# Performance work log

Hardware: AMD Instinct MI355X
Metric: run time of the kernel (lower is better)

The kernel has to match this reference:

```python
import jax, jax.numpy as jnp
import numpy as np

N, E, D = 50000, 800000, 128

def setup_inputs() -> dict:
    key = jax.random.key(0)
    ks = jax.random.split(key, 8)
    x = jax.random.normal(ks[0], (N, D), dtype=jnp.float32)
    edge_index = jax.random.randint(ks[1], (2, E), 0, N, dtype=jnp.int64)
    s2 = 1.0 / np.sqrt(2 * D)
    s4 = 1.0 / np.sqrt(4 * D)
    s1 = 1.0 / np.sqrt(D)
    pre_W = jax.random.uniform(ks[2], (2 * D, D), jnp.float32, -s2, s2)   # pre MLP (1 layer)
    pre_b = jax.random.uniform(ks[3], (D,), jnp.float32, -s2, s2)
    post_W = jax.random.uniform(ks[4], (4 * D, D), jnp.float32, -s4, s4)  # post MLP (1 layer)
    post_b = jax.random.uniform(ks[5], (D,), jnp.float32, -s4, s4)
    lin_W = jax.random.uniform(ks[6], (D, D), jnp.float32, -s1, s1)       # final projection
    lin_b = jax.random.uniform(ks[7], (D,), jnp.float32, -s1, s1)
    return {"x": x, "edge_index": edge_index, "pre_W": pre_W, "pre_b": pre_b,
            "post_W": post_W, "post_b": post_b, "lin_W": lin_W, "lin_b": lin_b}

def reference(x, edge_index, pre_W, pre_b, post_W, post_b, lin_W, lin_b):
    n = x.shape[0]
    src, dst = edge_index[0], edge_index[1]  # message flows src -> dst (source_to_target)
    # message: pre MLP on concat(x_i=target, x_j=source)  [E, 2D] -> [E, D]
    h = jnp.concatenate([x[dst], x[src]], axis=-1)
    m = h @ pre_W + pre_b
    # multi-aggregator scatter: mean, max, sum over destination nodes
    s = jax.ops.segment_sum(m, dst, num_segments=n)
    cnt = jax.ops.segment_sum(jnp.ones((m.shape[0], 1), m.dtype), dst, num_segments=n)
    mean = s / jnp.maximum(cnt, 1.0)
    mx = jax.ops.segment_max(m, dst, num_segments=n)
    mx = jnp.where(cnt > 0, mx, 0.0)  # empty segments -> 0 (PyG fill)
    aggr = jnp.concatenate([mean, mx, s], axis=-1)  # order: mean, max, sum
    # update: post MLP on concat(x, aggr)  [N, 4D] -> [N, D], then final lin
    out = jnp.concatenate([x, aggr], axis=-1) @ post_W + post_b
    out = out @ lin_W + lin_b
    # wrapper: relu + dropout (eval mode -> identity)
    return jax.nn.relu(out)
```

## Files before the change

### kernel.cpp

```cpp
#include <hip/hip_runtime.h>
#include <float.h>

#define NN 50000
#define EE 800000
#define NBKT 196
#define T1 4096
#define CAP2 8192

typedef __attribute__((ext_vector_type(8))) short bf16x8;
typedef __attribute__((ext_vector_type(4))) float f32x4;
typedef unsigned short u16;
typedef unsigned int u32;

__device__ __forceinline__ u16 f2bf(float f) {
  u32 u = __builtin_bit_cast(u32, f);
  u32 r = (u + 0x7fffu + ((u >> 16) & 1u)) >> 16;
  return (u16)r;
}
__device__ __forceinline__ float bflo(u32 q) { return __builtin_bit_cast(float, q << 16); }
__device__ __forceinline__ float bfhi(u32 q) { return __builtin_bit_cast(float, q & 0xffff0000u); }

__global__ __launch_bounds__(256) void k_prep(const float* __restrict__ post_W,
    const float* __restrict__ post_b, const float* __restrict__ lin_W,
    const float* __restrict__ lin_b, const float* __restrict__ pre_W,
    u16* __restrict__ WpT, u16* __restrict__ WpqT, float* __restrict__ bp) {
  int idx = blockIdx.x * 256 + threadIdx.x;
  if (idx < 512 * 128) {
    int i = idx >> 7, j = idx & 127;
    float s = 0.f;
#pragma unroll 8
    for (int c = 0; c < 128; c++) s += post_W[i * 128 + c] * lin_W[c * 128 + j];
    WpT[j * 512 + i] = f2bf(s);
  } else if (idx < 512 * 128 + 256 * 128) {
    int u = idx - 512 * 128;
    int j = u >> 7, k = u & 127;
    float v = (j < 128) ? pre_W[k * 128 + j] : pre_W[(128 + k) * 128 + (j - 128)];
    WpqT[j * 128 + k] = f2bf(v);
  } else if (idx < 512 * 128 + 256 * 128 + 128) {
    int j = idx - (512 * 128 + 256 * 128);
    float s = lin_b[j];
    for (int c = 0; c < 128; c++) s += post_b[c] * lin_W[c * 128 + j];
    bp[j] = s;
  }
}

__global__ __launch_bounds__(256) void k_convert_x(const float* __restrict__ x,
                                                   u16* __restrict__ Xcat) {
  int tid = blockIdx.x * 256 + threadIdx.x;
  if (tid >= NN * 16) return;
  int row = tid >> 4;
  int col = (tid & 15) << 3;
  const float4 v0 = *(const float4*)(x + (size_t)row * 128 + col);
  const float4 v1 = *(const float4*)(x + (size_t)row * 128 + col + 4);
  u16 tmp[8] = {f2bf(v0.x), f2bf(v0.y), f2bf(v0.z), f2bf(v0.w),
                f2bf(v1.x), f2bf(v1.y), f2bf(v1.z), f2bf(v1.w)};
  *(bf16x8*)(Xcat + (size_t)row * 512 + col) = *(bf16x8*)tmp;
}

template <int KTOT, int LDA>
__device__ __forceinline__ void stage_tiles(const u16* __restrict__ A,
    const u16* __restrict__ BT, int row0, int n0, int k0,
    u16* __restrict__ As, u16* __restrict__ Bs, int t) {
#pragma unroll
  for (int it = 0; it < 4; ++it) {
    int c = t + it * 256;
    int row = c >> 3, ch = c & 7;
    int gr = row0 + row;
    bf16x8 v = {};
    if (gr < NN) v = *(const bf16x8*)(A + (size_t)gr * LDA + k0 + (ch << 3));
    *(bf16x8*)(As + row * 64 + ((ch ^ (row & 7)) << 3)) = v;
  }
#pragma unroll
  for (int it = 0; it < 4; ++it) {
    int c = t + it * 256;
    int n = c >> 3, ch = c & 7;
    bf16x8 v = *(const bf16x8*)(BT + (size_t)(n0 + n) * KTOT + k0 + (ch << 3));
    *(bf16x8*)(Bs + n * 64 + ((ch ^ (n & 7)) << 3)) = v;
  }
}

__device__ __forceinline__ bf16x8 ld_frag(const u16* __restrict__ S, int rowbase,
                                          int kk, int lane) {
  int r = rowbase + (lane & 15);
  int chunk = (kk >> 3) + (lane >> 4);
  int sw = chunk ^ (r & 7);
  return *(const bf16x8*)(S + r * 64 + (sw << 3));
}

__global__ __launch_bounds__(256) void k_gemm_pq(const u16* __restrict__ Xcat,
    const u16* __restrict__ WpqT, u16* __restrict__ PQb) {
  __shared__ u16 As[128 * 64];
  __shared__ u16 Bs[128 * 64];
  const int t = threadIdx.x;
  const int lane = t & 63, wid = t >> 6;
  const int wr = wid >> 1, wc = wid & 1;
  const int row0 = blockIdx.x * 128;
  const int n0 = blockIdx.y * 128;
  f32x4 acc[4][4] = {};
  for (int k0 = 0; k0 < 128; k0 += 64) {
    stage_tiles<128, 512>(Xcat, WpqT, row0, n0, k0, As, Bs, t);
    __syncthreads();
#pragma unroll
    for (int kk = 0; kk < 64; kk += 32) {
      bf16x8 af[4], bg[4];
#pragma unroll
      for (int m = 0; m < 4; ++m) af[m] = ld_frag(As, wr * 64 + m * 16, kk, lane);
#pragma unroll
      for (int n = 0; n < 4; ++n) bg[n] = ld_frag(Bs, wc * 64 + n * 16, kk, lane);
#pragma unroll
      for (int m = 0; m < 4; ++m)
#pragma unroll
        for (int n = 0; n < 4; ++n)
          acc[m][n] = __builtin_amdgcn_mfma_f32_16x16x32_bf16(af[m], bg[n], acc[m][n], 0, 0, 0);
    }
    __syncthreads();
  }
#pragma unroll
  for (int m = 0; m < 4; ++m) {
    int rb = row0 + wr * 64 + m * 16 + ((lane >> 4) << 2);
#pragma unroll
    for (int n = 0; n < 4; ++n) {
      int col = n0 + wc * 64 + n * 16 + (lane & 15);
#pragma unroll
      for (int r = 0; r < 4; ++r) {
        int row = rb + r;
        if (row < NN) PQb[(size_t)row * 256 + col] = f2bf(acc[m][n][r]);
      }
    }
  }
}

__global__ __launch_bounds__(256) void k_gemm_out(const u16* __restrict__ Xcat,
    const u16* __restrict__ WpT, const float* __restrict__ bp,
    float* __restrict__ out) {
  __shared__ u16 As[128 * 64];
  __shared__ u16 Bs[128 * 64];
  const int t = threadIdx.x;
  const int lane = t & 63, wid = t >> 6;
  const int wr = wid >> 1, wc = wid & 1;
  const int row0 = blockIdx.x * 128;
  f32x4 acc[4][4] = {};
  for (int k0 = 0; k0 < 512; k0 += 64) {
    stage_tiles<512, 512>(Xcat, WpT, row0, 0, k0, As, Bs, t);
    __syncthreads();
#pragma unroll
    for (int kk = 0; kk < 64; kk += 32) {
      bf16x8 af[4], bg[4];
#pragma unroll
      for (int m = 0; m < 4; ++m) af[m] = ld_frag(As, wr * 64 + m * 16, kk, lane);
#pragma unroll
      for (int n = 0; n < 4; ++n) bg[n] = ld_frag(Bs, wc * 64 + n * 16, kk, lane);
#pragma unroll
      for (int m = 0; m < 4; ++m)
#pragma unroll
        for (int n = 0; n < 4; ++n)
          acc[m][n] = __builtin_amdgcn_mfma_f32_16x16x32_bf16(af[m], bg[n], acc[m][n], 0, 0, 0);
    }
    __syncthreads();
  }
#pragma unroll
  for (int m = 0; m < 4; ++m) {
    int rb = row0 + wr * 64 + m * 16 + ((lane >> 4) << 2);
#pragma unroll
    for (int n = 0; n < 4; ++n) {
      int col = wc * 64 + n * 16 + (lane & 15);
      float bias = bp[col];
#pragma unroll
      for (int r = 0; r < 4; ++r) {
        int row = rb + r;
        if (row < NN) out[(size_t)row * 128 + col] = fmaxf(acc[m][n][r] + bias, 0.f);
      }
    }
  }
}

__global__ void k_zero256(int* __restrict__ bucket_cnt) {
  bucket_cnt[threadIdx.x] = 0;
}

__global__ __launch_bounds__(256) void k_bucketcnt(const int* __restrict__ ei,
                                                   int* __restrict__ bucket_cnt) {
  __shared__ int hist[256];
  const int t = threadIdx.x;
  hist[t] = 0;
  __syncthreads();
  const int e0 = blockIdx.x * T1;
  const int ec = min(T1, EE - e0);
  for (int j = t; j < ec; j += 256) atomicAdd(&hist[ei[EE + e0 + j] >> 8], 1);
  __syncthreads();
  if (hist[t]) atomicAdd(&bucket_cnt[t], hist[t]);
}

__global__ void k_scanbucket(const int* __restrict__ bucket_cnt,
                             int* __restrict__ bucket_base,
                             int* __restrict__ bucket_cursor) {
  __shared__ int sd[256];
  int t = threadIdx.x;
  int v = (t < NBKT) ? bucket_cnt[t] : 0;
  sd[t] = v;
  __syncthreads();
  for (int s = 1; s < 256; s <<= 1) {
    int tv = (t >= s) ? sd[t - s] : 0;
    __syncthreads();
    sd[t] += tv;
    __syncthreads();
  }
  int excl = sd[t] - v;
  bucket_base[t] = excl;
  bucket_cursor[t] = excl;
}

__global__ __launch_bounds__(256) void k_bucket(const int* __restrict__ ei,
    int* __restrict__ bucket_cursor, u32* __restrict__ ebuf) {
  __shared__ u32 tilebuf[T1];
  __shared__ u32 gpos[T1];
  __shared__ int hist[256], scan_[256], runbase[256], ctr[256];
  const int t = threadIdx.x;
  const int e0 = blockIdx.x * T1;
  const int ecount = min(T1, EE - e0);
  hist[t] = 0;
  __syncthreads();
  u32 myp[16];
  int myb[16];
#pragma unroll
  for (int k = 0; k < 16; ++k) {
    int idx = t + k * 256;
    myp[k] = 0; myb[k] = 0;
    if (idx < ecount) {
      int e = e0 + idx;
      int s = ei[e], d = ei[EE + e];
      myp[k] = ((u32)d << 16) | (u32)s;
      int b = d >> 8;
      myb[k] = b;
      atomicAdd(&hist[b], 1);
    }
  }
  __syncthreads();
  int v = hist[t];
  scan_[t] = v;
  __syncthreads();
  for (int s_ = 1; s_ < 256; s_ <<= 1) {
    int tv = (t >= s_) ? scan_[t - s_] : 0;
    __syncthreads();
    scan_[t] += tv;
    __syncthreads();
  }
  int excl = scan_[t] - v;
  __syncthreads();
  scan_[t] = excl;
  ctr[t] = 0;
  if (v > 0) runbase[t] = atomicAdd(&bucket_cursor[t], v);
  __syncthreads();
#pragma unroll
  for (int k = 0; k < 16; ++k) {
    int idx = t + k * 256;
    if (idx < ecount) {
      int b = myb[k];
      int l = atomicAdd(&ctr[b], 1);
      int slot = scan_[b] + l;
      tilebuf[slot] = myp[k];
      gpos[slot] = (u32)(runbase[b] + l);
    }
  }
  __syncthreads();
  for (int j = t; j < ecount; j += 256) ebuf[gpos[j]] = tilebuf[j];
}

__global__ __launch_bounds__(256) void k_sortbucket(const u32* __restrict__ ebuf,
    const int* __restrict__ bucket_base, int* __restrict__ row_ptr,
    u16* __restrict__ csr_src) {
  __shared__ u16 sorted[CAP2];
  __shared__ int hist[256], scan_[256], ctr[256];
  const int b = blockIdx.x;
  const int t = threadIdx.x;
  const int base = bucket_base[b];
  const int end = bucket_base[b + 1];
  const int count = end - base;
  hist[t] = 0;
  __syncthreads();
  for (int j = t; j < count; j += 256) atomicAdd(&hist[(ebuf[base + j] >> 16) & 255], 1);
  __syncthreads();
  int v = hist[t];
  scan_[t] = v;
  __syncthreads();
  for (int s_ = 1; s_ < 256; s_ <<= 1) {
    int tv = (t >= s_) ? scan_[t - s_] : 0;
    __syncthreads();
    scan_[t] += tv;
    __syncthreads();
  }
  int excl = scan_[t] - v;
  __syncthreads();
  scan_[t] = excl;
  ctr[t] = 0;
  int node = b * 256 + t;
  if (node < NN) row_ptr[node] = base + excl;
  if (b == NBKT - 1 && t == 0) row_ptr[NN] = EE;
  __syncthreads();
  if (count <= CAP2) {
    for (int j = t; j < count; j += 256) {
      u32 p = ebuf[base + j];
      int ln = (p >> 16) & 255;
      int l = atomicAdd(&ctr[ln], 1);
      sorted[scan_[ln] + l] = (u16)(p & 0xffffu);
    }
    __syncthreads();
    for (int j = t; j < count; j += 256) csr_src[base + j] = sorted[j];
  } else {
    for (int j = t; j < count; j += 256) {
      u32 p = ebuf[base + j];
      int ln = (p >> 16) & 255;
      int l = atomicAdd(&ctr[ln], 1);
      csr_src[base + scan_[ln] + l] = (u16)(p & 0xffffu);
    }
  }
}

__global__ __launch_bounds__(256) void k_aggr(const u16* __restrict__ PQb,
    const float* __restrict__ pre_b, const int* __restrict__ row_ptr,
    const u16* __restrict__ csr_src, u16* __restrict__ Xcat) {
  int wid = (blockIdx.x * 256 + threadIdx.x) >> 6;
  int lane = threadIdx.x & 63;
  if (wid >= NN) return;
  int r0 = row_ptr[wid], r1 = row_ptr[wid + 1];
  int c = lane * 2;
  const u16* Qbase = PQb + 128 + c;
  float sx = 0.f, sy = 0.f, mxx = -FLT_MAX, mxy = -FLT_MAX;
  int i = r0;
  for (; i + 16 <= r1; i += 16) {
    int s[16];
#pragma unroll
    for (int k = 0; k < 16; ++k) s[k] = csr_src[i + k];
    u32 q[16];
#pragma unroll
    for (int k = 0; k < 16; ++k) q[k] = *(const u32*)(Qbase + (size_t)s[k] * 256);
#pragma unroll
    for (int k = 0; k < 16; ++k) {
      float qx = bflo(q[k]), qy = bfhi(q[k]);
      sx += qx; sy += qy;
      mxx = fmaxf(mxx, qx); mxy = fmaxf(mxy, qy);
    }
  }
  if (i + 8 <= r1) {
    int s[8];
#pragma unroll
    for (int k = 0; k < 8; ++k) s[k] = csr_src[i + k];
    u32 q[8];
#pragma unroll
    for (int k = 0; k < 8; ++k) q[k] = *(const u32*)(Qbase + (size_t)s[k] * 256);
#pragma unroll
    for (int k = 0; k < 8; ++k) {
      float qx = bflo(q[k]), qy = bfhi(q[k]);
      sx += qx; sy += qy;
      mxx = fmaxf(mxx, qx); mxy = fmaxf(mxy, qy);
    }
    i += 8;
  }
  if (i + 4 <= r1) {
    int s[4];
#pragma unroll
    for (int k = 0; k < 4; ++k) s[k] = csr_src[i + k];
    u32 q[4];
#pragma unroll
    for (int k = 0; k < 4; ++k) q[k] = *(const u32*)(Qbase + (size_t)s[k] * 256);
#pragma unroll
    for (int k = 0; k < 4; ++k) {
      float qx = bflo(q[k]), qy = bfhi(q[k]);
      sx += qx; sy += qy;
      mxx = fmaxf(mxx, qx); mxy = fmaxf(mxy, qy);
    }
    i += 4;
  }
  for (; i < r1; ++i) {
    int s = csr_src[i];
    u32 q = *(const u32*)(Qbase + (size_t)s * 256);
    float qx = bflo(q), qy = bfhi(q);
    sx += qx; sy += qy;
    mxx = fmaxf(mxx, qx); mxy = fmaxf(mxy, qy);
  }
  u32 pu = *(const u32*)(PQb + (size_t)wid * 256 + c);
  float2 b = *(const float2*)(pre_b + c);
  float px = bflo(pu) + b.x;
  float py = bfhi(pu) + b.y;
  int deg = r1 - r0;
  float vm_x = 0.f, vm_y = 0.f, vx_x = 0.f, vx_y = 0.f, vs_x = 0.f, vs_y = 0.f;
  if (deg > 0) {
    float inv = 1.0f / (float)deg;
    vm_x = px + sx * inv;          vm_y = py + sy * inv;
    vx_x = px + mxx;               vx_y = py + mxy;
    vs_x = (float)deg * px + sx;   vs_y = (float)deg * py + sy;
  }
  u16* arow = Xcat + (size_t)wid * 512 + 128;
  *(u32*)(arow + c)       = (u32)f2bf(vm_x) | ((u32)f2bf(vm_y) << 16);
  *(u32*)(arow + 128 + c) = (u32)f2bf(vx_x) | ((u32)f2bf(vx_y) << 16);
  *(u32*)(arow + 256 + c) = (u32)f2bf(vs_x) | ((u32)f2bf(vs_y) << 16);
}

extern "C" void kernel_launch(void* const* d_in, const int* in_sizes, int n_in,
                              void* d_out, int out_size, void* d_ws, size_t ws_size,
                              hipStream_t stream) {
  const float* x      = (const float*)d_in[0];
  const int*   ei     = (const int*)d_in[1];
  const float* pre_W  = (const float*)d_in[2];
  const float* pre_b  = (const float*)d_in[3];
  const float* post_W = (const float*)d_in[4];
  const float* post_b = (const float*)d_in[5];
  const float* lin_W  = (const float*)d_in[6];
  const float* lin_b  = (const float*)d_in[7];
  float* out = (float*)d_out;

  char* ws = (char*)d_ws;
  size_t off = 0;
  auto alloc = [&](size_t bytes) { size_t o = off; off = (off + bytes + 511) & ~(size_t)511; return o; };
  u16*   Xcat    = (u16*)(ws + alloc((size_t)NN * 512 * 2));
  u16*   PQb     = (u16*)(ws + alloc((size_t)NN * 256 * 2));
  u16*   WpT     = (u16*)(ws + alloc(128 * 512 * 2));
  u16*   WpqT    = (u16*)(ws + alloc(256 * 128 * 2));
  float* bp      = (float*)(ws + alloc(128 * 4));
  int*   row_ptr = (int*)(ws + alloc((size_t)(NN + 1) * 4));
  int*   bucket_cnt    = (int*)(ws + alloc(256 * 4));
  int*   bucket_base   = (int*)(ws + alloc(257 * 4));
  int*   bucket_cursor = (int*)(ws + alloc(256 * 4));
  u32*   ebuf    = (u32*)(ws + alloc((size_t)EE * 4));
  u16*   csr_src = (u16*)(ws + alloc((size_t)EE * 2));
  (void)ws_size; (void)in_sizes; (void)n_in; (void)out_size;

  const int NB_M = (NN + 127) / 128;
  const int NB_T = (EE + T1 - 1) / T1;

  k_prep<<<(512 * 128 + 256 * 128 + 128 + 255) / 256, 256, 0, stream>>>(
      post_W, post_b, lin_W, lin_b, pre_W, WpT, WpqT, bp);
  k_convert_x<<<(NN * 16 + 255) / 256, 256, 0, stream>>>(x, Xcat);
  k_zero256<<<1, 256, 0, stream>>>(bucket_cnt);
  k_bucketcnt<<<NB_T, 256, 0, stream>>>(ei, bucket_cnt);
  k_gemm_pq<<<dim3(NB_M, 2), 256, 0, stream>>>(Xcat, WpqT, PQb);
  k_scanbucket<<<1, 256, 0, stream>>>(bucket_cnt, bucket_base, bucket_cursor);
  k_bucket<<<NB_T, 256, 0, stream>>>(ei, bucket_cursor, ebuf);
  k_sortbucket<<<NBKT, 256, 0, stream>>>(ebuf, bucket_base, row_ptr, csr_src);
  k_aggr<<<(NN * 64 + 255) / 256, 256, 0, stream>>>(PQb, pre_b, row_ptr, csr_src, Xcat);
  k_gemm_out<<<NB_M, 256, 0, stream>>>(Xcat, WpT, bp, out);
}
```

Measured before the change: 126.6 us.

## Fuse setup kernels, use per-tile bucket partials, smaller out-GEMM tiles, scalarize CSR indices

Measured after the change: 127.0 us. Within noise of the previous version (+0.3%).

```diff
diff --git a/kernel.cpp b/kernel.cpp
--- a/kernel.cpp
+++ b/kernel.cpp
@@ -7,6 +7,11 @@
 #define T1 4096
 #define CAP2 8192
 
+#define NB_CONV 3125
+#define NB_PREP 385
+#define NB_CNT  196
+#define NB_SETUP (NB_CONV + NB_PREP + NB_CNT)
+
 typedef __attribute__((ext_vector_type(8))) short bf16x8;
 typedef __attribute__((ext_vector_type(4))) float f32x4;
 typedef unsigned short u16;
@@ -20,49 +25,188 @@
 __device__ __forceinline__ float bflo(u32 q) { return __builtin_bit_cast(float, q << 16); }
 __device__ __forceinline__ float bfhi(u32 q) { return __builtin_bit_cast(float, q & 0xffff0000u); }
 
-__global__ __launch_bounds__(256) void k_prep(const float* __restrict__ post_W,
-    const float* __restrict__ post_b, const float* __restrict__ lin_W,
-    const float* __restrict__ lin_b, const float* __restrict__ pre_W,
-    u16* __restrict__ WpT, u16* __restrict__ WpqT, float* __restrict__ bp) {
-  int idx = blockIdx.x * 256 + threadIdx.x;
-  if (idx < 512 * 128) {
-    int i = idx >> 7, j = idx & 127;
-    float s = 0.f;
+__global__ __launch_bounds__(256) void k_setup(const float* __restrict__ x,
+    const float* __restrict__ post_W, const float* __restrict__ post_b,
+    const float* __restrict__ lin_W, const float* __restrict__ lin_b,
+    const float* __restrict__ pre_W, const int* __restrict__ ei,
+    u16* __restrict__ Xcat, u16* __restrict__ WpT, u16* __restrict__ WpqT,
+    float* __restrict__ bp, int* __restrict__ bucket_part) {
+  __shared__ int hist[256];
+  const int bid = blockIdx.x;
+  const int t = threadIdx.x;
+  if (bid < NB_CONV) {
+    int tid = bid * 256 + t;
+    int row = tid >> 4;
+    int col = (tid & 15) << 3;
+    const float4 v0 = *(const float4*)(x + (size_t)row * 128 + col);
+    const float4 v1 = *(const float4*)(x + (size_t)row * 128 + col + 4);
+    u16 tmp[8] = {f2bf(v0.x), f2bf(v0.y), f2bf(v0.z), f2bf(v0.w),
+                  f2bf(v1.x), f2bf(v1.y), f2bf(v1.z), f2bf(v1.w)};
+    *(bf16x8*)(Xcat + (size_t)row * 512 + col) = *(bf16x8*)tmp;
+  } else if (bid < NB_CONV + NB_PREP) {
+    int idx = (bid - NB_CONV) * 256 + t;
+    if (idx < 512 * 128) {
+      int i = idx >> 7, j = idx & 127;
+      float s = 0.f;
 #pragma unroll 8
-    for (int c = 0; c < 128; c++) s += post_W[i * 128 + c] * lin_W[c * 128 + j];
-    WpT[j * 512 + i] = f2bf(s);
-  } else if (idx < 512 * 128 + 256 * 128) {
-    int u = idx - 512 * 128;
-    int j = u >> 7, k = u & 127;
-    float v = (j < 128) ? pre_W[k * 128 + j] : pre_W[(128 + k) * 128 + (j - 128)];
-    WpqT[j * 128 + k] = f2bf(v);
-  } else if (idx < 512 * 128 + 256 * 128 + 128) {
-    int j = idx - (512 * 128 + 256 * 128);
-    float s = lin_b[j];
-    for (int c = 0; c < 128; c++) s += post_b[c] * lin_W[c * 128 + j];
-    bp[j] = s;
-  }
-}
-
-__global__ __launch_bounds__(256) void k_convert_x(const float* __restrict__ x,
-                                                   u16* __restrict__ Xcat) {
-  int tid = blockIdx.x * 256 + threadIdx.x;
-  if (tid >= NN * 16) return;
-  int row = tid >> 4;
-  int col = (tid & 15) << 3;
-  const float4 v0 = *(const float4*)(x + (size_t)row * 128 + col);
-  const float4 v1 = *(const float4*)(x + (size_t)row * 128 + col + 4);
-  u16 tmp[8] = {f2bf(v0.x), f2bf(v0.y), f2bf(v0.z), f2bf(v0.w),
-                f2bf(v1.x), f2bf(v1.y), f2bf(v1.z), f2bf(v1.w)};
-  *(bf16x8*)(Xcat + (size_t)row * 512 + col) = *(bf16x8*)tmp;
-}
-
-template <int KTOT, int LDA>
+      for (int c = 0; c < 128; c++) s += post_W[i * 128 + c] * lin_W[c * 128 + j];
+      WpT[j * 512 + i] = f2bf(s);
+    } else if (idx < 512 * 128 + 256 * 128) {
+      int u = idx - 512 * 128;
+      int j = u >> 7, k = u & 127;
+      float v = (j < 128) ? pre_W[k * 128 + j] : pre_W[(128 + k) * 128 + (j - 128)];
+      WpqT[j * 128 + k] = f2bf(v);
+    } else if (idx < 512 * 128 + 256 * 128 + 128) {
+      int j = idx - (512 * 128 + 256 * 128);
+      float s = lin_b[j];
+      for (int c = 0; c < 128; c++) s += post_b[c] * lin_W[c * 128 + j];
+      bp[j] = s;
+    }
+  } else {
+    int tile = bid - (NB_CONV + NB_PREP);
+    hist[t] = 0;
+    __syncthreads();
+    const int e0 = tile * T1;
+    const int ec = min(T1, EE - e0);
+    for (int j = t; j < ec; j += 256) atomicAdd(&hist[ei[EE + e0 + j] >> 8], 1);
+    __syncthreads();
+    bucket_part[tile * 256 + t] = hist[t];
+  }
+}
+
+__global__ void k_scanbucket(const int* __restrict__ bucket_part,
+                             int* __restrict__ bucket_base,
+                             int* __restrict__ bucket_cursor) {
+  __shared__ int sd[256];
+  int t = threadIdx.x;
+  int v = 0;
+#pragma unroll 4
+  for (int b = 0; b < NB_CNT; ++b) v += bucket_part[b * 256 + t];
+  sd[t] = v;
+  __syncthreads();
+  for (int s = 1; s < 256; s <<= 1) {
+    int tv = (t >= s) ? sd[t - s] : 0;
+    __syncthreads();
+    sd[t] += tv;
+    __syncthreads();
+  }
+  int excl = sd[t] - v;
+  bucket_base[t] = excl;
+  bucket_cursor[t] = excl;
+}
+
+__global__ __launch_bounds__(256) void k_bucket(const int* __restrict__ ei,
+    int* __restrict__ bucket_cursor, u32* __restrict__ ebuf) {
+  __shared__ u32 tilebuf[T1];
+  __shared__ u32 gpos[T1];
+  __shared__ int hist[256], scan_[256], runbase[256], ctr[256];
+  const int t = threadIdx.x;
+  const int e0 = blockIdx.x * T1;
+  const int ecount = min(T1, EE - e0);
+  hist[t] = 0;
+  __syncthreads();
+  u32 myp[16];
+  int myb[16];
+#pragma unroll
+  for (int k = 0; k < 16; ++k) {
+    int idx = t + k * 256;
+    myp[k] = 0; myb[k] = 0;
+    if (idx < ecount) {
+      int e = e0 + idx;
+      int s = ei[e], d = ei[EE + e];
+      myp[k] = ((u32)d << 16) | (u32)s;
+      int b = d >> 8;
+      myb[k] = b;
+      atomicAdd(&hist[b], 1);
+    }
+  }
+  __syncthreads();
+  int v = hist[t];
+  scan_[t] = v;
+  __syncthreads();
+  for (int s_ = 1; s_ < 256; s_ <<= 1) {
+    int tv = (t >= s_) ? scan_[t - s_] : 0;
+    __syncthreads();
+    scan_[t] += tv;
+    __syncthreads();
+  }
+  int excl = scan_[t] - v;
+  __syncthreads();
+  scan_[t] = excl;
+  ctr[t] = 0;
+  if (v > 0) runbase[t] = atomicAdd(&bucket_cursor[t], v);
+  __syncthreads();
+#pragma unroll
+  for (int k = 0; k < 16; ++k) {
+    int idx = t + k * 256;
+    if (idx < ecount) {
+      int b = myb[k];
+      int l = atomicAdd(&ctr[b], 1);
+      int slot = scan_[b] + l;
+      tilebuf[slot] = myp[k];
+      gpos[slot] = (u32)(runbase[b] + l);
+    }
+  }
+  __syncthreads();
+  for (int j = t; j < ecount; j += 256) ebuf[gpos[j]] = tilebuf[j];
+}
+
+__global__ __launch_bounds__(256) void k_sortbucket(const u32* __restrict__ ebuf,
+    const int* __restrict__ bucket_base, int* __restrict__ row_ptr,
+    u16* __restrict__ csr_src) {
+  __shared__ u16 sorted[CAP2];
+  __shared__ int hist[256], scan_[256], ctr[256];
+  const int b = blockIdx.x;
+  const int t = threadIdx.x;
+  const int base = bucket_base[b];
+  const int end = bucket_base[b + 1];
+  const int count = end - base;
+  hist[t] = 0;
+  __syncthreads();
+  for (int j = t; j < count; j += 256) atomicAdd(&hist[(ebuf[base + j] >> 16) & 255], 1);
+  __syncthreads();
+  int v = hist[t];
+  scan_[t] = v;
+  __syncthreads();
+  for (int s_ = 1; s_ < 256; s_ <<= 1) {
+    int tv = (t >= s_) ? scan_[t - s_] : 0;
+    __syncthreads();
+    scan_[t] += tv;
+    __syncthreads();
+  }
+  int excl = scan_[t] - v;
+  __syncthreads();
+  scan_[t] = excl;
+  ctr[t] = 0;
+  int node = b * 256 + t;
+  if (node < NN) row_ptr[node] = base + excl;
+  if (b == NBKT - 1 && t == 0) row_ptr[NN] = EE;
+  __syncthreads();
+  if (count <= CAP2) {
+    for (int j = t; j < count; j += 256) {
+      u32 p = ebuf[base + j];
+      int ln = (p >> 16) & 255;
+      int l = atomicAdd(&ctr[ln], 1);
+      sorted[scan_[ln] + l] = (u16)(p & 0xffffu);
+    }
+    __syncthreads();
+    for (int j = t; j < count; j += 256) csr_src[base + j] = sorted[j];
+  } else {
+    for (int j = t; j < count; j += 256) {
+      u32 p = ebuf[base + j];
+      int ln = (p >> 16) & 255;
+      int l = atomicAdd(&ctr[ln], 1);
+      csr_src[base + scan_[ln] + l] = (u16)(p & 0xffffu);
+    }
+  }
+}
+
+template <int KTOT, int LDA, int AROWS>
 __device__ __forceinline__ void stage_tiles(const u16* __restrict__ A,
     const u16* __restrict__ BT, int row0, int n0, int k0,
     u16* __restrict__ As, u16* __restrict__ Bs, int t) {
 #pragma unroll
-  for (int it = 0; it < 4; ++it) {
+  for (int it = 0; it < AROWS / 32; ++it) {
     int c = t + it * 256;
     int row = c >> 3, ch = c & 7;
     int gr = row0 + row;
@@ -98,7 +242,7 @@
   const int n0 = blockIdx.y * 128;
   f32x4 acc[4][4] = {};
   for (int k0 = 0; k0 < 128; k0 += 64) {
-    stage_tiles<128, 512>(Xcat, WpqT, row0, n0, k0, As, Bs, t);
+    stage_tiles<128, 512, 128>(Xcat, WpqT, row0, n0, k0, As, Bs, t);
     __syncthreads();
 #pragma unroll
     for (int kk = 0; kk < 64; kk += 32) {
@@ -133,25 +277,25 @@
 __global__ __launch_bounds__(256) void k_gemm_out(const u16* __restrict__ Xcat,
     const u16* __restrict__ WpT, const float* __restrict__ bp,
     float* __restrict__ out) {
-  __shared__ u16 As[128 * 64];
+  __shared__ u16 As[64 * 64];
   __shared__ u16 Bs[128 * 64];
   const int t = threadIdx.x;
   const int lane = t & 63, wid = t >> 6;
   const int wr = wid >> 1, wc = wid & 1;
-  const int row0 = blockIdx.x * 128;
-  f32x4 acc[4][4] = {};
+  const int row0 = blockIdx.x * 64;
+  f32x4 acc[2][4] = {};
   for (int k0 = 0; k0 < 512; k0 += 64) {
-    stage_tiles<512, 512>(Xcat, WpT, row0, 0, k0, As, Bs, t);
+    stage_tiles<512, 512, 64>(Xcat, WpT, row0, 0, k0, As, Bs, t);
     __syncthreads();
 #pragma unroll
     for (int kk = 0; kk < 64; kk += 32) {
-      bf16x8 af[4], bg[4];
-#pragma unroll
-      for (int m = 0; m < 4; ++m) af[m] = ld_frag(As, wr * 64 + m * 16, kk, lane);
+      bf16x8 af[2], bg[4];
+#pragma unroll
+      for (int m = 0; m < 2; ++m) af[m] = ld_frag(As, wr * 32 + m * 16, kk, lane);
 #pragma unroll
       for (int n = 0; n < 4; ++n) bg[n] = ld_frag(Bs, wc * 64 + n * 16, kk, lane);
 #pragma unroll
-      for (int m = 0; m < 4; ++m)
+      for (int m = 0; m < 2; ++m)
 #pragma unroll
         for (int n = 0; n < 4; ++n)
           acc[m][n] = __builtin_amdgcn_mfma_f32_16x16x32_bf16(af[m], bg[n], acc[m][n], 0, 0, 0);
@@ -159,8 +303,8 @@
     __syncthreads();
   }
 #pragma unroll
-  for (int m = 0; m < 4; ++m) {
-    int rb = row0 + wr * 64 + m * 16 + ((lane >> 4) << 2);
+  for (int m = 0; m < 2; ++m) {
+    int rb = row0 + wr * 32 + m * 16 + ((lane >> 4) << 2);
 #pragma unroll
     for (int n = 0; n < 4; ++n) {
       int col = wc * 64 + n * 16 + (lane & 15);
@@ -170,148 +314,6 @@
         int row = rb + r;
         if (row < NN) out[(size_t)row * 128 + col] = fmaxf(acc[m][n][r] + bias, 0.f);
       }
-    }
-  }
-}
-
-__global__ void k_zero256(int* __restrict__ bucket_cnt) {
-  bucket_cnt[threadIdx.x] = 0;
-}
-
-__global__ __launch_bounds__(256) void k_bucketcnt(const int* __restrict__ ei,
-                                                   int* __restrict__ bucket_cnt) {
-  __shared__ int hist[256];
-  const int t = threadIdx.x;
-  hist[t] = 0;
-  __syncthreads();
-  const int e0 = blockIdx.x * T1;
-  const int ec = min(T1, EE - e0);
-  for (int j = t; j < ec; j += 256) atomicAdd(&hist[ei[EE + e0 + j] >> 8], 1);
-  __syncthreads();
-  if (hist[t]) atomicAdd(&bucket_cnt[t], hist[t]);
-}
-
-__global__ void k_scanbucket(const int* __restrict__ bucket_cnt,
-                             int* __restrict__ bucket_base,
-                             int* __restrict__ bucket_cursor) {
-  __shared__ int sd[256];
-  int t = threadIdx.x;
-  int v = (t < NBKT) ? bucket_cnt[t] : 0;
-  sd[t] = v;
-  __syncthreads();
-  for (int s = 1; s < 256; s <<= 1) {
-    int tv = (t >= s) ? sd[t - s] : 0;
-    __syncthreads();
-    sd[t] += tv;
-    __syncthreads();
-  }
-  int excl = sd[t] - v;
-  bucket_base[t] = excl;
-  bucket_cursor[t] = excl;
-}
-
-__global__ __launch_bounds__(256) void k_bucket(const int* __restrict__ ei,
-    int* __restrict__ bucket_cursor, u32* __restrict__ ebuf) {
-  __shared__ u32 tilebuf[T1];
-  __shared__ u32 gpos[T1];
-  __shared__ int hist[256], scan_[256], runbase[256], ctr[256];
-  const int t = threadIdx.x;
-  const int e0 = blockIdx.x * T1;
-  const int ecount = min(T1, EE - e0);
-  hist[t] = 0;
-  __syncthreads();
-  u32 myp[16];
-  int myb[16];
-#pragma unroll
-  for (int k = 0; k < 16; ++k) {
-    int idx = t + k * 256;
-    myp[k] = 0; myb[k] = 0;
-    if (idx < ecount) {
-      int e = e0 + idx;
-      int s = ei[e], d = ei[EE + e];
-      myp[k] = ((u32)d << 16) | (u32)s;
-      int b = d >> 8;
-      myb[k] = b;
-      atomicAdd(&hist[b], 1);
-    }
-  }
-  __syncthreads();
-  int v = hist[t];
-  scan_[t] = v;
-  __syncthreads();
-  for (int s_ = 1; s_ < 256; s_ <<= 1) {
-    int tv = (t >= s_) ? scan_[t - s_] : 0;
-    __syncthreads();
-    scan_[t] += tv;
-    __syncthreads();
-  }
-  int excl = scan_[t] - v;
-  __syncthreads();
-  scan_[t] = excl;
-  ctr[t] = 0;
-  if (v > 0) runbase[t] = atomicAdd(&bucket_cursor[t], v);
-  __syncthreads();
-#pragma unroll
-  for (int k = 0; k < 16; ++k) {
-    int idx = t + k * 256;
-    if (idx < ecount) {
-      int b = myb[k];
-      int l = atomicAdd(&ctr[b], 1);
-      int slot = scan_[b] + l;
-      tilebuf[slot] = myp[k];
-      gpos[slot] = (u32)(runbase[b] + l);
-    }
-  }
-  __syncthreads();
-  for (int j = t; j < ecount; j += 256) ebuf[gpos[j]] = tilebuf[j];
-}
-
-__global__ __launch_bounds__(256) void k_sortbucket(const u32* __restrict__ ebuf,
-    const int* __restrict__ bucket_base, int* __restrict__ row_ptr,
-    u16* __restrict__ csr_src) {
-  __shared__ u16 sorted[CAP2];
-  __shared__ int hist[256], scan_[256], ctr[256];
-  const int b = blockIdx.x;
-  const int t = threadIdx.x;
-  const int base = bucket_base[b];
-  const int end = bucket_base[b + 1];
-  const int count = end - base;
-  hist[t] = 0;
-  __syncthreads();
-  for (int j = t; j < count; j += 256) atomicAdd(&hist[(ebuf[base + j] >> 16) & 255], 1);
-  __syncthreads();
-  int v = hist[t];
-  scan_[t] = v;
-  __syncthreads();
-  for (int s_ = 1; s_ < 256; s_ <<= 1) {
-    int tv = (t >= s_) ? scan_[t - s_] : 0;
-    __syncthreads();
-    scan_[t] += tv;
-    __syncthreads();
-  }
-  int excl = scan_[t] - v;
-  __syncthreads();
-  scan_[t] = excl;
-  ctr[t] = 0;
-  int node = b * 256 + t;
-  if (node < NN) row_ptr[node] = base + excl;
-  if (b == NBKT - 1 && t == 0) row_ptr[NN] = EE;
-  __syncthreads();
-  if (count <= CAP2) {
-    for (int j = t; j < count; j += 256) {
-      u32 p = ebuf[base + j];
-      int ln = (p >> 16) & 255;
-      int l = atomicAdd(&ctr[ln], 1);
-      sorted[scan_[ln] + l] = (u16)(p & 0xffffu);
-    }
-    __syncthreads();
-    for (int j = t; j < count; j += 256) csr_src[base + j] = sorted[j];
-  } else {
-    for (int j = t; j < count; j += 256) {
-      u32 p = ebuf[base + j];
-      int ln = (p >> 16) & 255;
-      int l = atomicAdd(&ctr[ln], 1);
-      csr_src[base + scan_[ln] + l] = (u16)(p & 0xffffu);
     }
   }
 }
@@ -322,7 +324,8 @@
   int wid = (blockIdx.x * 256 + threadIdx.x) >> 6;
   int lane = threadIdx.x & 63;
   if (wid >= NN) return;
-  int r0 = row_ptr[wid], r1 = row_ptr[wid + 1];
+  int r0 = __builtin_amdgcn_readfirstlane(row_ptr[wid]);
+  int r1 = __builtin_amdgcn_readfirstlane(row_ptr[wid + 1]);
   int c = lane * 2;
   const u16* Qbase = PQb + 128 + c;
   float sx = 0.f, sy = 0.f, mxx = -FLT_MAX, mxy = -FLT_MAX;
@@ -330,7 +333,7 @@
   for (; i + 16 <= r1; i += 16) {
     int s[16];
 #pragma unroll
-    for (int k = 0; k < 16; ++k) s[k] = csr_src[i + k];
+    for (int k = 0; k < 16; ++k) s[k] = __builtin_amdgcn_readfirstlane((int)csr_src[i + k]);
     u32 q[16];
 #pragma unroll
     for (int k = 0; k < 16; ++k) q[k] = *(const u32*)(Qbase + (size_t)s[k] * 256);
@@ -344,7 +347,7 @@
   if (i + 8 <= r1) {
     int s[8];
 #pragma unroll
-    for (int k = 0; k < 8; ++k) s[k] = csr_src[i + k];
+    for (int k = 0; k < 8; ++k) s[k] = __builtin_amdgcn_readfirstlane((int)csr_src[i + k]);
     u32 q[8];
 #pragma unroll
     for (int k = 0; k < 8; ++k) q[k] = *(const u32*)(Qbase + (size_t)s[k] * 256);
@@ -359,7 +362,7 @@
   if (i + 4 <= r1) {
     int s[4];
 #pragma unroll
-    for (int k = 0; k < 4; ++k) s[k] = csr_src[i + k];
+    for (int k = 0; k < 4; ++k) s[k] = __builtin_amdgcn_readfirstlane((int)csr_src[i + k]);
     u32 q[4];
 #pragma unroll
     for (int k = 0; k < 4; ++k) q[k] = *(const u32*)(Qbase + (size_t)s[k] * 256);
@@ -372,7 +375,7 @@
     i += 4;
   }
   for (; i < r1; ++i) {
-    int s = csr_src[i];
+    int s = __builtin_amdgcn_readfirstlane((int)csr_src[i]);
     u32 q = *(const u32*)(Qbase + (size_t)s * 256);
     float qx = bflo(q), qy = bfhi(q);
     sx += qx; sy += qy;
@@ -418,7 +421,7 @@
   u16*   WpqT    = (u16*)(ws + alloc(256 * 128 * 2));
   float* bp      = (float*)(ws + alloc(128 * 4));
   int*   row_ptr = (int*)(ws + alloc((size_t)(NN + 1) * 4));
-  int*   bucket_cnt    = (int*)(ws + alloc(256 * 4));
+  int*   bucket_part   = (int*)(ws + alloc((size_t)NB_CNT * 256 * 4));
   int*   bucket_base   = (int*)(ws + alloc(257 * 4));
   int*   bucket_cursor = (int*)(ws + alloc(256 * 4));
   u32*   ebuf    = (u32*)(ws + alloc((size_t)EE * 4));
@@ -426,17 +429,14 @@
   (void)ws_size; (void)in_sizes; (void)n_in; (void)out_size;
 
   const int NB_M = (NN + 127) / 128;
-  const int NB_T = (EE + T1 - 1) / T1;
-
-  k_prep<<<(512 * 128 + 256 * 128 + 128 + 255) / 256, 256, 0, stream>>>(
-      post_W, post_b, lin_W, lin_b, pre_W, WpT, WpqT, bp);
-  k_convert_x<<<(NN * 16 + 255) / 256, 256, 0, stream>>>(x, Xcat);
-  k_zero256<<<1, 256, 0, stream>>>(bucket_cnt);
-  k_bucketcnt<<<NB_T, 256, 0, stream>>>(ei, bucket_cnt);
+  const int NB_M64 = (NN + 63) / 64;
+
+  k_setup<<<NB_SETUP, 256, 0, stream>>>(x, post_W, post_b, lin_W, lin_b, pre_W, ei,
+                                        Xcat, WpT, WpqT, bp, bucket_part);
+  k_scanbucket<<<1, 256, 0, stream>>>(bucket_part, bucket_base, bucket_cursor);
+  k_bucket<<<NB_CNT, 256, 0, stream>>>(ei, bucket_cursor, ebuf);
+  k_sortbucket<<<NBKT, 256, 0, stream>>>(ebuf, bucket_base, row_ptr, csr_src);
   k_gemm_pq<<<dim3(NB_M, 2), 256, 0, stream>>>(Xcat, WpqT, PQb);
-  k_scanbucket<<<1, 256, 0, stream>>>(bucket_cnt, bucket_base, bucket_cursor);
-  k_bucket<<<NB_T, 256, 0, stream>>>(ei, bucket_cursor, ebuf);
-  k_sortbucket<<<NBKT, 256, 0, stream>>>(ebuf, bucket_base, row_ptr, csr_src);
   k_aggr<<<(NN * 64 + 255) / 256, 256, 0, stream>>>(PQb, pre_b, row_ptr, csr_src, Xcat);
-  k_gemm_out<<<NB_M, 256, 0, stream>>>(Xcat, WpT, bp, out);
-}
+  k_gemm_out<<<NB_M64, 256, 0, stream>>>(Xcat, WpT, bp, out);
+}
```
